# Performance work log

Measured on AMD Instinct MI355X. Metric: run time of the kernel, lower is better.

## Reference

```python
import jax, jax.numpy as jnp
import numpy as np

THRESH_LOW = 0.90
THRESH_HIGH = 0.95
IOU_THRESH = 0.05
IOU_LOW = 0.1


def _interp1d(size, dtype):
    # roi_align sample offsets for a 4-wide box, bin=4, grid=ceil(4/1)=4:
    # center + (i+0.5)*1 - 2 -> {-1.5,-0.5,0.5,1.5}
    offs = jnp.array([-1.5, -0.5, 0.5, 1.5], dtype)
    c = jnp.arange(size, dtype=dtype)[:, None] + offs  # [size,4]
    valid = (c >= -1.0) & (c <= size)  # torchvision: zero if y < -1 or y > H
    cc = jnp.clip(c, 0.0, size - 1.0)
    lo = jnp.floor(cc).astype(jnp.int32)
    hi = jnp.minimum(lo + 1, size - 1)
    frac = cc - lo.astype(dtype)
    w_lo = jnp.where(valid, 1.0 - frac, 0.0)
    w_hi = jnp.where(valid, frac, 0.0)
    return lo, hi, w_lo, w_hi


def _roi_pool(m):
    # roi_align(output_size=1, spatial_scale=1, sampling_ratio=-1, aligned=False)
    # over one 4x4 anchor per pixel: separable bilinear gather, mean of 16 samples.
    H, W = m.shape
    ylo, yhi, wy0, wy1 = _interp1d(H, m.dtype)
    xlo, xhi, wx0, wx1 = _interp1d(W, m.dtype)
    A = jnp.einsum('hkw,hk->hw', m[ylo], wy0) + jnp.einsum('hkw,hk->hw', m[yhi], wy1)
    B = jnp.einsum('hwk,wk->hw', A[:, xlo], wx0) + jnp.einsum('hwk,wk->hw', A[:, xhi], wx1)
    return B / 16.0


def _anchors(H, W, dtype):
    # torchvision AnchorGenerator(sizes=(5,), aspects=(1.0,)): base anchor
    # round([-2.5,-2.5,2.5,2.5]) = [-2,-2,2,2]; stride 1; x fastest, y outer.
    yy, xx = jnp.meshgrid(jnp.arange(H, dtype=dtype), jnp.arange(W, dtype=dtype), indexing='ij')
    a = jnp.stack([xx - 2.0, yy - 2.0, xx + 2.0, yy + 2.0], axis=-1)
    return a.reshape(-1, 4)


def _iou_one_vs_all(box, boxes):
    lt = jnp.maximum(box[:2], boxes[:, :2])
    rb = jnp.minimum(box[2:], boxes[:, 2:])
    wh = jnp.maximum(rb - lt, 0.0)
    inter = wh[:, 0] * wh[:, 1]
    area1 = (box[2] - box[0]) * (box[3] - box[1])
    area2 = (boxes[:, 2] - boxes[:, 0]) * (boxes[:, 3] - boxes[:, 1])
    return inter / (area1 + area2 - inter)


def _nms(boxes, scores, thr):
    # Greedy NMS (torchvision semantics: suppress IoU > thr), returns kept
    # indices sorted by descending score. Row-wise IoU avoids an MxM matrix.
    M = boxes.shape[0]
    if M == 0:
        return jnp.zeros((0,), jnp.int32)
    order = jnp.argsort(-scores)
    b = boxes[order]
    rng = jnp.arange(M)
    def body(i, keep):
        sup = (_iou_one_vs_all(b[i], b) > thr) & (rng > i) & keep[i]
        return keep & ~sup
    keep = jax.lax.fori_loop(0, M, body, jnp.ones((M,), bool))
    return order[keep]


def _logits(x1, x2, x3):
    r = (jnp.abs(x1 - x2).sum(axis=1) + jnp.abs(x2 - x3).sum(axis=1)) / 2.0  # [B,H,W]
    rmax = r.reshape(r.shape[0], -1).max(axis=-1)[:, None, None]
    rmin = r.reshape(r.shape[0], -1).min(axis=-1)[:, None, None]
    r = (r - rmin) / (rmax - rmin + 1e-6)
    m = r[0]  # B == 1
    logits = _roi_pool(m).reshape(-1)  # [H*W], row-major (y outer, x inner)
    return logits / (logits.max() + 1e-6)


def setup_inputs():
    key = jax.random.key(0)
    k1, k2, k3 = jax.random.split(key, 3)
    shape = (1, 8, 1024, 1024)
    return {
        'x1': jax.random.normal(k1, shape, jnp.float32),
        'x2': jax.random.normal(k2, shape, jnp.float32),
        'x3': jax.random.normal(k3, shape, jnp.float32),
    }


def reference(x1, x2, x3):
    H, W = x1.shape[-2:]
    anchors = _anchors(H, W, x1.dtype)
    logits = _logits(x1, x2, x3)
    idx = jnp.arange(logits.shape[0])
    # low band, NMS @ 0.1
    idx_low = idx[(logits > THRESH_LOW) & (logits < THRESH_HIGH)]
    idx_low = idx_low[_nms(anchors[idx_low], logits[idx_low], IOU_LOW)]
    # high band, NMS @ iou_thresh
    idx_high = idx[logits > THRESH_HIGH]
    idx_high = idx_high[_nms(anchors[idx_high], logits[idx_high], IOU_THRESH)]
    # combined NMS
    idx_cat = jnp.concatenate([idx_high, idx_low])
    idx_final = idx_cat[_nms(anchors[idx_cat], logits[idx_cat], IOU_THRESH)]
    return jnp.concatenate([anchors[idx_final], logits[idx_final][:, None]], axis=-1)
```

## Files before the change

### kernel.cpp

```cpp
#include <hip/hip_runtime.h>
#include <stdint.h>

#define GW 1024
#define GH 1024
#define NPIX (GW*GH)
#define CAP 8192
#define ADJ_STRIDE 48

__global__ void k_resid(const float4* __restrict__ x1, const float4* __restrict__ x2,
                        const float4* __restrict__ x3, float4* __restrict__ r,
                        float2* __restrict__ pmm) {
  const int N4 = NPIX / 4;
  int t = blockIdx.x * blockDim.x + threadIdx.x;
  float4 s1 = make_float4(0.f,0.f,0.f,0.f);
  float4 s2 = make_float4(0.f,0.f,0.f,0.f);
#pragma unroll
  for (int c = 0; c < 8; ++c) {
    float4 a = x1[c*N4 + t];
    float4 b = x2[c*N4 + t];
    float4 d = x3[c*N4 + t];
    s1.x += fabsf(a.x-b.x); s1.y += fabsf(a.y-b.y);
    s1.z += fabsf(a.z-b.z); s1.w += fabsf(a.w-b.w);
    s2.x += fabsf(b.x-d.x); s2.y += fabsf(b.y-d.y);
    s2.z += fabsf(b.z-d.z); s2.w += fabsf(b.w-d.w);
  }
  float4 rv = make_float4((s1.x+s2.x)*0.5f, (s1.y+s2.y)*0.5f,
                          (s1.z+s2.z)*0.5f, (s1.w+s2.w)*0.5f);
  r[t] = rv;
  float mn = fminf(fminf(rv.x,rv.y), fminf(rv.z,rv.w));
  float mx = fmaxf(fmaxf(rv.x,rv.y), fmaxf(rv.z,rv.w));
#pragma unroll
  for (int o = 32; o > 0; o >>= 1) {
    mn = fminf(mn, __shfl_down(mn, o));
    mx = fmaxf(mx, __shfl_down(mx, o));
  }
  __shared__ float smn[4], smx[4];
  int wid = threadIdx.x >> 6;
  if ((threadIdx.x & 63) == 0) { smn[wid] = mn; smx[wid] = mx; }
  __syncthreads();
  if (threadIdx.x == 0) {
    float a = fminf(fminf(smn[0], smn[1]), fminf(smn[2], smn[3]));
    float b = fmaxf(fmaxf(smx[0], smx[1]), fmaxf(smx[2], smx[3]));
    pmm[blockIdx.x] = make_float2(a, b);
  }
}

__global__ __launch_bounds__(1024) void k_reduce1(const float2* __restrict__ pmm,
                                                  unsigned int* __restrict__ mm) {
  int t = threadIdx.x;
  float2 p = pmm[t];
  float mn = p.x, mx = p.y;
#pragma unroll
  for (int o = 32; o > 0; o >>= 1) {
    mn = fminf(mn, __shfl_down(mn, o));
    mx = fmaxf(mx, __shfl_down(mx, o));
  }
  __shared__ float smn[16], smx[16];
  int wid = t >> 6;
  if ((t & 63) == 0) { smn[wid] = mn; smx[wid] = mx; }
  __syncthreads();
  if (t == 0) {
    mn = smn[0]; mx = smx[0];
#pragma unroll
    for (int i = 1; i < 16; ++i) { mn = fminf(mn, smn[i]); mx = fmaxf(mx, smx[i]); }
    mm[1] = __float_as_uint(mn);
    mm[2] = __float_as_uint(mx);
  }
}

__global__ void k_convy(const float* __restrict__ r, float* __restrict__ A,
                        const unsigned int* __restrict__ mm) {
  int x = blockIdx.x * 256 + threadIdx.x;
  int y = blockIdx.y;
  float rmin = __uint_as_float(mm[1]);
  float denom = __uint_as_float(mm[2]) - rmin + 1e-6f;
  const float offs[4] = {-1.5f, -0.5f, 0.5f, 1.5f};
  float a = 0.f, b = 0.f;
#pragma unroll
  for (int k = 0; k < 4; ++k) {
    float c = (float)y + offs[k];
    bool valid = (c >= -1.0f) && (c <= (float)GH);
    float cc = fminf(fmaxf(c, 0.0f), (float)(GH - 1));
    int lo = (int)floorf(cc);
    int hi = min(lo + 1, GH - 1);
    float frac = cc - (float)lo;
    float w0 = valid ? 1.0f - frac : 0.0f;
    float w1 = valid ? frac : 0.0f;
    a += ((r[lo*GW + x] - rmin) / denom) * w0;
    b += ((r[hi*GW + x] - rmin) / denom) * w1;
  }
  A[y*GW + x] = a + b;
}

__global__ void k_convx(const float* __restrict__ A, float* __restrict__ B,
                        float* __restrict__ pbmax) {
  __shared__ float sA[GW];
  __shared__ float smx[4];
  int y = blockIdx.x, t = threadIdx.x;
  ((float4*)sA)[t] = ((const float4*)(A + (size_t)y*GW))[t];
  __syncthreads();
  const float offs[4] = {-1.5f, -0.5f, 0.5f, 1.5f};
  float mxv = 0.0f;
#pragma unroll
  for (int q = 0; q < 4; ++q) {
    int x = t + 256*q;
    float a = 0.f, b = 0.f;
#pragma unroll
    for (int k = 0; k < 4; ++k) {
      float c = (float)x + offs[k];
      bool valid = (c >= -1.0f) && (c <= (float)GW);
      float cc = fminf(fmaxf(c, 0.0f), (float)(GW - 1));
      int lo = (int)floorf(cc);
      int hi = min(lo + 1, GW - 1);
      float frac = cc - (float)lo;
      float w0 = valid ? 1.0f - frac : 0.0f;
      float w1 = valid ? frac : 0.0f;
      a += sA[lo] * w0;
      b += sA[hi] * w1;
    }
    float v = (a + b) * 0.0625f;
    B[(size_t)y*GW + x] = v;
    mxv = fmaxf(mxv, v);
  }
#pragma unroll
  for (int o = 32; o > 0; o >>= 1) mxv = fmaxf(mxv, __shfl_down(mxv, o));
  int wid = t >> 6;
  if ((t & 63) == 0) smx[wid] = mxv;
  __syncthreads();
  if (t == 0)
    pbmax[y] = fmaxf(fmaxf(smx[0], smx[1]), fmaxf(smx[2], smx[3]));
}

__global__ __launch_bounds__(1024) void k_reduce2(const float* __restrict__ pbmax,
                                                  unsigned int* __restrict__ mm) {
  int t = threadIdx.x;
  float mx = pbmax[t];
#pragma unroll
  for (int o = 32; o > 0; o >>= 1) mx = fmaxf(mx, __shfl_down(mx, o));
  __shared__ float smx[16];
  int wid = t >> 6;
  if ((t & 63) == 0) smx[wid] = mx;
  __syncthreads();
  if (t == 0) {
    mx = smx[0];
#pragma unroll
    for (int i = 1; i < 16; ++i) mx = fmaxf(mx, smx[i]);
    mm[3] = __float_as_uint(mx);
    mm[0] = 0u;
    mm[4] = 0u;
  }
}

__global__ void k_cand(const float4* __restrict__ B, uint4* __restrict__ map,
                       unsigned int* __restrict__ list, unsigned int* __restrict__ mm) {
  int t = blockIdx.x * 256 + threadIdx.x;
  int tid = threadIdx.x;
  float bmax = __uint_as_float(mm[3]);
  float dv = bmax + 1e-6f;
  float4 b = B[t];
  map[t] = make_uint4(~0u, ~0u, ~0u, ~0u);
  float l[4] = { b.x/dv, b.y/dv, b.z/dv, b.w/dv };
  unsigned int flags = 0; int cnt = 0;
#pragma unroll
  for (int k = 0; k < 4; ++k) {
    float s = l[k];
    if (s > 0.90f && !(s == 0.95f)) { flags |= 1u << k; cnt++; }
  }
  __shared__ unsigned int sscan[256];
  __shared__ unsigned int sbase;
  sscan[tid] = (unsigned int)cnt;
  __syncthreads();
  for (int off = 1; off < 256; off <<= 1) {
    unsigned int v = sscan[tid];
    unsigned int a = (tid >= off) ? sscan[tid - off] : 0u;
    __syncthreads();
    sscan[tid] = v + a;
    __syncthreads();
  }
  if (tid == 255) {
    unsigned int tot = sscan[255];
    if (tot) sbase = atomicAdd(&mm[0], tot);
  }
  __syncthreads();
  if (flags) {
    unsigned int o = sbase + sscan[tid] - (unsigned int)cnt;
    unsigned int base4 = (unsigned int)t * 4u;
#pragma unroll
    for (int k = 0; k < 4; ++k) {
      if ((flags >> k) & 1u) {
        if (o < CAP) list[o] = base4 + (unsigned int)k;
        o++;
      }
    }
  }
}

__global__ __launch_bounds__(1024) void k_sort(const float* __restrict__ B,
                                               const unsigned int* __restrict__ list,
                                               unsigned int* __restrict__ map,
                                               unsigned int* __restrict__ mm,
                                               unsigned long long* __restrict__ keysOut) {
  __shared__ unsigned long long keys[CAP];
  __shared__ unsigned int s_high;
  const int tid = threadIdx.x;
  if (tid == 0) s_high = 0;
  __syncthreads();
  int M = (int)min(mm[0], (unsigned int)CAP);
  unsigned int P = 2;
  while (P < (unsigned int)M) P <<= 1;
  float bmax = __uint_as_float(mm[3]);
  unsigned int hc = 0;
  for (unsigned int i = tid; i < P; i += 1024) {
    unsigned long long k = ~0ULL;
    if ((int)i < M) {
      unsigned int pos = list[i];
      float s = B[pos] / (bmax + 1e-6f);
      unsigned int sb = __float_as_uint(s);
      k = (((unsigned long long)(0xFFFFFFFFu - sb)) << 32) | (unsigned long long)pos;
      if (s > 0.95f) hc++;
    }
    keys[i] = k;
  }
  if (hc) atomicAdd(&s_high, hc);
  __syncthreads();
  for (unsigned int kk = 2; kk <= P; kk <<= 1) {
    for (unsigned int j = kk >> 1; j > 0; j >>= 1) {
      for (unsigned int i = tid; i < P; i += 1024) {
        unsigned int ixj = i ^ j;
        if (ixj > i) {
          unsigned long long a = keys[i], b = keys[ixj];
          bool asc = ((i & kk) == 0);
          if (asc ? (a > b) : (a < b)) { keys[i] = b; keys[ixj] = a; }
        }
      }
      __syncthreads();
    }
  }
  for (unsigned int i = tid; i < P; i += 1024) {
    unsigned long long k = keys[i];
    keysOut[i] = k;
    if ((int)i < M) map[(unsigned int)(k & 0xFFFFFFFFu)] = i;
  }
  if (tid == 0) mm[4] = s_high;
}

__global__ void k_adj(const unsigned long long* __restrict__ keys,
                      const unsigned int* __restrict__ map,
                      const unsigned int* __restrict__ mm,
                      unsigned short* __restrict__ adj) {
  int r = blockIdx.x * 256 + threadIdx.x;
  int M = (int)min(mm[0], (unsigned int)CAP);
  if (r >= M) return;
  unsigned int pos = (unsigned int)(keys[r] & 0xFFFFFFFFu);
  int y = (int)(pos >> 10), x = (int)(pos & 1023);
  int n = 0, n3 = 0;
  unsigned short* row = adj + (size_t)r * ADJ_STRIDE;
#pragma unroll
  for (int pass = 0; pass < 2; ++pass) {
    for (int dy = -3; dy <= 3; ++dy) {
      int ady = dy < 0 ? -dy : dy;
      int wy = 4 - ady;
      int ny = y + dy;
      if ((unsigned)ny >= (unsigned)GH) continue;
      for (int dx = -3; dx <= 3; ++dx) {
        if ((dx | dy) == 0) continue;
        int adx = dx < 0 ? -dx : dx;
        int prod = (4 - adx) * wy;
        if (prod < 2) continue;
        if ((pass == 0) != (prod >= 3)) continue;
        int nx = x + dx;
        if ((unsigned)nx >= (unsigned)GW) continue;
        unsigned int nrk = map[ny*GW + nx];
        if (nrk < (unsigned int)r) {
          row[1 + n] = (unsigned short)nrk;
          n++;
          if (pass == 0) n3++;
        }
      }
    }
  }
  row[0] = (unsigned short)(n3 | (n << 8));
}

__global__ __launch_bounds__(1024) void k_nms(const unsigned long long* __restrict__ keys,
                                              const unsigned short* __restrict__ adj,
                                              const unsigned int* __restrict__ mm,
                                              float* __restrict__ out, int nrows) {
  __shared__ unsigned char st[CAP];
  __shared__ unsigned short act[2][CAP];
  __shared__ unsigned int s_cnt[2];
  __shared__ unsigned int scan[1024];
  const int tid = threadIdx.x;
  int M = (int)min(mm[0], (unsigned int)CAP);
  int nH = (int)mm[4];
  for (int i = tid; i < CAP; i += 1024) st[i] = 0;
  for (int i = tid; i < M; i += 1024) act[0][i] = (unsigned short)i;
  if (tid == 0) { s_cnt[0] = (unsigned int)M; s_cnt[1] = 0; }
  __syncthreads();

  int cur = 0;
  for (int round = 0; round < CAP; ++round) {
    unsigned int cnt = s_cnt[cur];
    if (cnt == 0) break;
    for (unsigned int i = tid; i < cnt; i += 1024) {
      int r = act[cur][i];
      bool high = r < nH;
      const unsigned short* row = adj + (size_t)r * ADJ_STRIDE;
      unsigned int hdr = row[0];
      int n = high ? (int)(hdr >> 8) : (int)(hdr & 0xFF);
      bool sup = false, und = false;
      for (int k = 1; k <= n; ++k) {
        int p = row[k];
        if ((p < nH) != high) continue;
        unsigned char ps = st[p];
        if (ps & 2) { sup = true; break; }
        if (!(ps & 1)) und = true;
      }
      if (sup)          st[r] = 1;
      else if (!und)    st[r] = 3;
      else { unsigned int j = atomicAdd(&s_cnt[cur ^ 1], 1u); act[cur ^ 1][j] = (unsigned short)r; }
    }
    __syncthreads();
    if (tid == 0) s_cnt[cur] = 0;
    cur ^= 1;
    __syncthreads();
  }
  __syncthreads();

  if (tid == 0) { s_cnt[0] = 0; s_cnt[1] = 0; }
  __syncthreads();
  for (int i = nH + tid; i < M; i += 1024)
    if (st[i] & 2) { unsigned int j = atomicAdd(&s_cnt[0], 1u); act[0][j] = (unsigned short)i; }
  __syncthreads();
  cur = 0;
  for (int round = 0; round < CAP; ++round) {
    unsigned int cnt = s_cnt[cur];
    if (cnt == 0) break;
    for (unsigned int i = tid; i < cnt; i += 1024) {
      int r = act[cur][i];
      const unsigned short* row = adj + (size_t)r * ADJ_STRIDE;
      unsigned int hdr = row[0];
      int n = (int)(hdr >> 8);
      bool sup = false, und = false;
      for (int k = 1; k <= n; ++k) {
        int p = row[k];
        unsigned char ps = st[p];
        if (p < nH) {
          if (ps & 2) { sup = true; break; }
        } else {
          if (!(ps & 2)) continue;
          if (ps & 8) { sup = true; break; }
          if (!(ps & 4)) und = true;
        }
      }
      if (sup)          st[r] |= 4;
      else if (!und)    st[r] |= 12;
      else { unsigned int j = atomicAdd(&s_cnt[cur ^ 1], 1u); act[cur ^ 1][j] = (unsigned short)r; }
    }
    __syncthreads();
    if (tid == 0) s_cnt[cur] = 0;
    cur ^= 1;
    __syncthreads();
  }
  __syncthreads();

  int base = tid * 8;
  int cnt = 0;
  unsigned int flags = 0;
#pragma unroll
  for (int k = 0; k < 8; ++k) {
    int r = base + k;
    bool keep = false;
    if (r < M) keep = (r < nH) ? ((st[r] & 2) != 0) : ((st[r] & 8) != 0);
    if (keep) { flags |= 1u << k; cnt++; }
  }
  scan[tid] = (unsigned int)cnt;
  __syncthreads();
  for (int off = 1; off < 1024; off <<= 1) {
    unsigned int v = scan[tid];
    unsigned int a = (tid >= off) ? scan[tid - off] : 0u;
    __syncthreads();
    scan[tid] = v + a;
    __syncthreads();
  }
  unsigned int off0 = scan[tid] - (unsigned int)cnt;
  int w = 0;
#pragma unroll
  for (int k = 0; k < 8; ++k) {
    if (flags & (1u << k)) {
      int r = base + k;
      unsigned int j = off0 + (unsigned int)w; w++;
      if ((int)j < nrows) {
        unsigned long long kv = keys[r];
        unsigned int pos = (unsigned int)(kv & 0xFFFFFFFFu);
        float s = __uint_as_float(0xFFFFFFFFu - (unsigned int)(kv >> 32));
        float fx = (float)(pos & 1023), fy = (float)(pos >> 10);
        out[j*5 + 0] = fx - 2.0f;
        out[j*5 + 1] = fy - 2.0f;
        out[j*5 + 2] = fx + 2.0f;
        out[j*5 + 3] = fy + 2.0f;
        out[j*5 + 4] = s;
      }
    }
  }
}

extern "C" void kernel_launch(void* const* d_in, const int* in_sizes, int n_in,
                              void* d_out, int out_size, void* d_ws, size_t ws_size,
                              hipStream_t stream) {
  const float* x1 = (const float*)d_in[0];
  const float* x2 = (const float*)d_in[1];
  const float* x3 = (const float*)d_in[2];
  char* ws = (char*)d_ws;
  float* rmap = (float*)ws;
  float* Amap = (float*)(ws + (4u << 20));
  float* Bmap = (float*)(ws + (8u << 20));
  unsigned int* map = (unsigned int*)(ws + (4u << 20));
  unsigned int* mm  = (unsigned int*)(ws + (12u << 20));
  unsigned int* list = (unsigned int*)(ws + (12u << 20) + 4096u);
  unsigned long long* keys = (unsigned long long*)(ws + (12u << 20) + (64u << 10));
  unsigned short* adj = (unsigned short*)(ws + (12u << 20) + (128u << 10));
  float2* pmm = (float2*)(ws + (13u << 20));
  float* pbmax = (float*)(ws + (13u << 20) + (16u << 10));
  float* out = (float*)d_out;

  k_resid<<<NPIX/4/256, 256, 0, stream>>>((const float4*)x1, (const float4*)x2,
                                          (const float4*)x3, (float4*)rmap, pmm);
  k_reduce1<<<1, 1024, 0, stream>>>(pmm, mm);
  dim3 g2(GW/256, GH);
  k_convy<<<g2, 256, 0, stream>>>(rmap, Amap, mm);
  k_convx<<<GH, 256, 0, stream>>>(Amap, Bmap, pbmax);
  k_reduce2<<<1, 1024, 0, stream>>>(pbmax, mm);
  k_cand<<<NPIX/4/256, 256, 0, stream>>>((const float4*)Bmap, (uint4*)map, list, mm);
  k_sort<<<1, 1024, 0, stream>>>(Bmap, list, map, mm, keys);
  k_adj<<<CAP/256, 256, 0, stream>>>(keys, map, mm, adj);
  k_nms<<<1, 1024, 0, stream>>>(keys, adj, mm, out, out_size / 5);
}
```

Measured before the change: 216.8 us.

## Drop full candidate bitonic sort; compare scores in adjacency and rank-sort only kept boxes

Removes the single-block bitonic sort over all candidates (up to 8192 keys). Candidate scores and map indices are now written directly in k_cand. k_adj decides suppression priority by comparing neighbour scores and positions, and it packs a high/low band flag into each adjacency entry and the row header. At the end, only the surviving boxes are ordered by an O(K^2) rank count in shared memory. This saves one kernel launch and the long serial sort. The costs are a quadratic final ranking, a 4096 cap on kept boxes, and narrower 6-bit neighbour counts.

```diff
diff --git a/kernel.cpp b/kernel.cpp
--- a/kernel.cpp
+++ b/kernel.cpp
@@ -5,6 +5,7 @@
 #define GH 1024
 #define NPIX (GW*GH)
 #define CAP 8192
+#define KCAP 4096
 #define ADJ_STRIDE 48
 
 __global__ void k_resid(const float4* __restrict__ x1, const float4* __restrict__ x2,
@@ -147,18 +148,17 @@
     for (int i = 1; i < 16; ++i) mx = fmaxf(mx, smx[i]);
     mm[3] = __float_as_uint(mx);
     mm[0] = 0u;
-    mm[4] = 0u;
   }
 }
 
 __global__ void k_cand(const float4* __restrict__ B, uint4* __restrict__ map,
-                       unsigned int* __restrict__ list, unsigned int* __restrict__ mm) {
+                       unsigned int* __restrict__ list, float* __restrict__ scores,
+                       unsigned int* __restrict__ mm) {
   int t = blockIdx.x * 256 + threadIdx.x;
   int tid = threadIdx.x;
   float bmax = __uint_as_float(mm[3]);
   float dv = bmax + 1e-6f;
   float4 b = B[t];
-  map[t] = make_uint4(~0u, ~0u, ~0u, ~0u);
   float l[4] = { b.x/dv, b.y/dv, b.z/dv, b.w/dv };
   unsigned int flags = 0; int cnt = 0;
 #pragma unroll
@@ -182,76 +182,33 @@
     if (tot) sbase = atomicAdd(&mm[0], tot);
   }
   __syncthreads();
+  unsigned int mv[4] = { ~0u, ~0u, ~0u, ~0u };
   if (flags) {
     unsigned int o = sbase + sscan[tid] - (unsigned int)cnt;
     unsigned int base4 = (unsigned int)t * 4u;
 #pragma unroll
     for (int k = 0; k < 4; ++k) {
       if ((flags >> k) & 1u) {
-        if (o < CAP) list[o] = base4 + (unsigned int)k;
+        if (o < CAP) { list[o] = base4 + (unsigned int)k; scores[o] = l[k]; mv[k] = o; }
         o++;
       }
     }
   }
-}
-
-__global__ __launch_bounds__(1024) void k_sort(const float* __restrict__ B,
-                                               const unsigned int* __restrict__ list,
-                                               unsigned int* __restrict__ map,
-                                               unsigned int* __restrict__ mm,
-                                               unsigned long long* __restrict__ keysOut) {
-  __shared__ unsigned long long keys[CAP];
-  __shared__ unsigned int s_high;
-  const int tid = threadIdx.x;
-  if (tid == 0) s_high = 0;
-  __syncthreads();
-  int M = (int)min(mm[0], (unsigned int)CAP);
-  unsigned int P = 2;
-  while (P < (unsigned int)M) P <<= 1;
-  float bmax = __uint_as_float(mm[3]);
-  unsigned int hc = 0;
-  for (unsigned int i = tid; i < P; i += 1024) {
-    unsigned long long k = ~0ULL;
-    if ((int)i < M) {
-      unsigned int pos = list[i];
-      float s = B[pos] / (bmax + 1e-6f);
-      unsigned int sb = __float_as_uint(s);
-      k = (((unsigned long long)(0xFFFFFFFFu - sb)) << 32) | (unsigned long long)pos;
-      if (s > 0.95f) hc++;
-    }
-    keys[i] = k;
-  }
-  if (hc) atomicAdd(&s_high, hc);
-  __syncthreads();
-  for (unsigned int kk = 2; kk <= P; kk <<= 1) {
-    for (unsigned int j = kk >> 1; j > 0; j >>= 1) {
-      for (unsigned int i = tid; i < P; i += 1024) {
-        unsigned int ixj = i ^ j;
-        if (ixj > i) {
-          unsigned long long a = keys[i], b = keys[ixj];
-          bool asc = ((i & kk) == 0);
-          if (asc ? (a > b) : (a < b)) { keys[i] = b; keys[ixj] = a; }
-        }
-      }
-      __syncthreads();
-    }
-  }
-  for (unsigned int i = tid; i < P; i += 1024) {
-    unsigned long long k = keys[i];
-    keysOut[i] = k;
-    if ((int)i < M) map[(unsigned int)(k & 0xFFFFFFFFu)] = i;
-  }
-  if (tid == 0) mm[4] = s_high;
-}
-
-__global__ void k_adj(const unsigned long long* __restrict__ keys,
+  map[t] = make_uint4(mv[0], mv[1], mv[2], mv[3]);
+}
+
+__global__ void k_adj(const unsigned int* __restrict__ list,
+                      const float* __restrict__ scores,
                       const unsigned int* __restrict__ map,
                       const unsigned int* __restrict__ mm,
                       unsigned short* __restrict__ adj) {
   int r = blockIdx.x * 256 + threadIdx.x;
   int M = (int)min(mm[0], (unsigned int)CAP);
   if (r >= M) return;
-  unsigned int pos = (unsigned int)(keys[r] & 0xFFFFFFFFu);
+  unsigned int pos = list[r];
+  float s = scores[r];
+  unsigned int sb = __float_as_uint(s);
+  unsigned int high = (s > 0.95f) ? 1u : 0u;
   int y = (int)(pos >> 10), x = (int)(pos & 1023);
   int n = 0, n3 = 0;
   unsigned short* row = adj + (size_t)r * ADJ_STRIDE;
@@ -270,32 +227,38 @@
         if ((pass == 0) != (prod >= 3)) continue;
         int nx = x + dx;
         if ((unsigned)nx >= (unsigned)GW) continue;
-        unsigned int nrk = map[ny*GW + nx];
-        if (nrk < (unsigned int)r) {
-          row[1 + n] = (unsigned short)nrk;
+        unsigned int npix = (unsigned int)(ny*GW + nx);
+        unsigned int nid = map[npix];
+        if (nid == ~0u) continue;
+        float ns = scores[nid];
+        unsigned int nsb = __float_as_uint(ns);
+        if (nsb > sb || (nsb == sb && npix < pos)) {
+          unsigned int nh = (ns > 0.95f) ? 1u : 0u;
+          row[1 + n] = (unsigned short)(nid | (nh << 15));
           n++;
           if (pass == 0) n3++;
         }
       }
     }
   }
-  row[0] = (unsigned short)(n3 | (n << 8));
-}
-
-__global__ __launch_bounds__(1024) void k_nms(const unsigned long long* __restrict__ keys,
+  row[0] = (unsigned short)(n3 | (n << 6) | (high << 12));
+}
+
+__global__ __launch_bounds__(1024) void k_nms(const unsigned int* __restrict__ list,
+                                              const float* __restrict__ scores,
                                               const unsigned short* __restrict__ adj,
                                               const unsigned int* __restrict__ mm,
                                               float* __restrict__ out, int nrows) {
   __shared__ unsigned char st[CAP];
   __shared__ unsigned short act[2][CAP];
+  __shared__ unsigned long long skeys[KCAP];
   __shared__ unsigned int s_cnt[2];
-  __shared__ unsigned int scan[1024];
+  __shared__ unsigned int s_k;
   const int tid = threadIdx.x;
   int M = (int)min(mm[0], (unsigned int)CAP);
-  int nH = (int)mm[4];
   for (int i = tid; i < CAP; i += 1024) st[i] = 0;
   for (int i = tid; i < M; i += 1024) act[0][i] = (unsigned short)i;
-  if (tid == 0) { s_cnt[0] = (unsigned int)M; s_cnt[1] = 0; }
+  if (tid == 0) { s_cnt[0] = (unsigned int)M; s_cnt[1] = 0; s_k = 0; }
   __syncthreads();
 
   int cur = 0;
@@ -304,20 +267,21 @@
     if (cnt == 0) break;
     for (unsigned int i = tid; i < cnt; i += 1024) {
       int r = act[cur][i];
-      bool high = r < nH;
       const unsigned short* row = adj + (size_t)r * ADJ_STRIDE;
       unsigned int hdr = row[0];
-      int n = high ? (int)(hdr >> 8) : (int)(hdr & 0xFF);
+      unsigned int high = (hdr >> 12) & 1u;
+      int n = high ? (int)((hdr >> 6) & 63u) : (int)(hdr & 63u);
+      unsigned char lowbit = high ? 0 : 16;
       bool sup = false, und = false;
       for (int k = 1; k <= n; ++k) {
-        int p = row[k];
-        if ((p < nH) != high) continue;
-        unsigned char ps = st[p];
+        unsigned int e = row[k];
+        if (((e >> 15) & 1u) != high) continue;
+        unsigned char ps = st[e & 0x1FFFu];
         if (ps & 2) { sup = true; break; }
         if (!(ps & 1)) und = true;
       }
-      if (sup)          st[r] = 1;
-      else if (!und)    st[r] = 3;
+      if (sup)          st[r] = (unsigned char)(1 | lowbit);
+      else if (!und)    st[r] = (unsigned char)(3 | lowbit);
       else { unsigned int j = atomicAdd(&s_cnt[cur ^ 1], 1u); act[cur ^ 1][j] = (unsigned short)r; }
     }
     __syncthreads();
@@ -329,8 +293,12 @@
 
   if (tid == 0) { s_cnt[0] = 0; s_cnt[1] = 0; }
   __syncthreads();
-  for (int i = nH + tid; i < M; i += 1024)
-    if (st[i] & 2) { unsigned int j = atomicAdd(&s_cnt[0], 1u); act[0][j] = (unsigned short)i; }
+  for (int i = tid; i < M; i += 1024) {
+    unsigned char s0 = st[i];
+    if ((s0 & 16) && (s0 & 2)) {
+      unsigned int j = atomicAdd(&s_cnt[0], 1u); act[0][j] = (unsigned short)i;
+    }
+  }
   __syncthreads();
   cur = 0;
   for (int round = 0; round < CAP; ++round) {
@@ -340,12 +308,12 @@
       int r = act[cur][i];
       const unsigned short* row = adj + (size_t)r * ADJ_STRIDE;
       unsigned int hdr = row[0];
-      int n = (int)(hdr >> 8);
+      int n = (int)((hdr >> 6) & 63u);
       bool sup = false, und = false;
       for (int k = 1; k <= n; ++k) {
-        int p = row[k];
-        unsigned char ps = st[p];
-        if (p < nH) {
+        unsigned int e = row[k];
+        unsigned char ps = st[e & 0x1FFFu];
+        if ((e >> 15) & 1u) {
           if (ps & 2) { sup = true; break; }
         } else {
           if (!(ps & 2)) continue;
@@ -364,43 +332,34 @@
   }
   __syncthreads();
 
-  int base = tid * 8;
-  int cnt = 0;
-  unsigned int flags = 0;
-#pragma unroll
-  for (int k = 0; k < 8; ++k) {
-    int r = base + k;
-    bool keep = false;
-    if (r < M) keep = (r < nH) ? ((st[r] & 2) != 0) : ((st[r] & 8) != 0);
-    if (keep) { flags |= 1u << k; cnt++; }
-  }
-  scan[tid] = (unsigned int)cnt;
-  __syncthreads();
-  for (int off = 1; off < 1024; off <<= 1) {
-    unsigned int v = scan[tid];
-    unsigned int a = (tid >= off) ? scan[tid - off] : 0u;
-    __syncthreads();
-    scan[tid] = v + a;
-    __syncthreads();
-  }
-  unsigned int off0 = scan[tid] - (unsigned int)cnt;
-  int w = 0;
-#pragma unroll
-  for (int k = 0; k < 8; ++k) {
-    if (flags & (1u << k)) {
-      int r = base + k;
-      unsigned int j = off0 + (unsigned int)w; w++;
-      if ((int)j < nrows) {
-        unsigned long long kv = keys[r];
-        unsigned int pos = (unsigned int)(kv & 0xFFFFFFFFu);
-        float s = __uint_as_float(0xFFFFFFFFu - (unsigned int)(kv >> 32));
-        float fx = (float)(pos & 1023), fy = (float)(pos >> 10);
-        out[j*5 + 0] = fx - 2.0f;
-        out[j*5 + 1] = fy - 2.0f;
-        out[j*5 + 2] = fx + 2.0f;
-        out[j*5 + 3] = fy + 2.0f;
-        out[j*5 + 4] = s;
-      }
+  for (int i = tid; i < M; i += 1024) {
+    unsigned char s0 = st[i];
+    bool keep = (s0 & 16) ? ((s0 & 8) != 0) : ((s0 & 2) != 0);
+    if (keep) {
+      unsigned int j = atomicAdd(&s_k, 1u);
+      if (j < KCAP) {
+        unsigned int pos = list[i];
+        unsigned int sb = __float_as_uint(scores[i]);
+        skeys[j] = (((unsigned long long)(0xFFFFFFFFu - sb)) << 32) | (unsigned long long)pos;
+      }
+    }
+  }
+  __syncthreads();
+  unsigned int K = min(s_k, (unsigned int)KCAP);
+
+  for (unsigned int i = tid; i < K; i += 1024) {
+    unsigned long long key = skeys[i];
+    unsigned int rank = 0;
+    for (unsigned int q = 0; q < K; ++q) rank += (skeys[q] < key) ? 1u : 0u;
+    if ((int)rank < nrows) {
+      unsigned int pos = (unsigned int)(key & 0xFFFFFFFFu);
+      float s = __uint_as_float(0xFFFFFFFFu - (unsigned int)(key >> 32));
+      float fx = (float)(pos & 1023), fy = (float)(pos >> 10);
+      out[rank*5 + 0] = fx - 2.0f;
+      out[rank*5 + 1] = fy - 2.0f;
+      out[rank*5 + 2] = fx + 2.0f;
+      out[rank*5 + 3] = fy + 2.0f;
+      out[rank*5 + 4] = s;
     }
   }
 }
@@ -418,7 +377,7 @@
   unsigned int* map = (unsigned int*)(ws + (4u << 20));
   unsigned int* mm  = (unsigned int*)(ws + (12u << 20));
   unsigned int* list = (unsigned int*)(ws + (12u << 20) + 4096u);
-  unsigned long long* keys = (unsigned long long*)(ws + (12u << 20) + (64u << 10));
+  float* scores = (float*)(ws + (12u << 20) + (64u << 10));
   unsigned short* adj = (unsigned short*)(ws + (12u << 20) + (128u << 10));
   float2* pmm = (float2*)(ws + (13u << 20));
   float* pbmax = (float*)(ws + (13u << 20) + (16u << 10));
@@ -431,8 +390,7 @@
   k_convy<<<g2, 256, 0, stream>>>(rmap, Amap, mm);
   k_convx<<<GH, 256, 0, stream>>>(Amap, Bmap, pbmax);
   k_reduce2<<<1, 1024, 0, stream>>>(pbmax, mm);
-  k_cand<<<NPIX/4/256, 256, 0, stream>>>((const float4*)Bmap, (uint4*)map, list, mm);
-  k_sort<<<1, 1024, 0, stream>>>(Bmap, list, map, mm, keys);
-  k_adj<<<CAP/256, 256, 0, stream>>>(keys, map, mm, adj);
-  k_nms<<<1, 1024, 0, stream>>>(keys, adj, mm, out, out_size / 5);
-}
+  k_cand<<<NPIX/4/256, 256, 0, stream>>>((const float4*)Bmap, (uint4*)map, list, scores, mm);
+  k_adj<<<CAP/256, 256, 0, stream>>>(list, scores, map, mm, adj);
+  k_nms<<<1, 1024, 0, stream>>>(list, scores, adj, mm, out, out_size / 5);
+}
```

Result: faster. 199.4 us (-8.0%).
